# Kernel optimization log

Hardware: AMD Instinct MI355X
Metric: run time of the kernel (lower is better)

Reference implementation:

```python
import jax, jax.numpy as jnp
import numpy as np

_W1 = np.array([[[-1, 0, 0], [0, 1, 0], [0, 0, 0]],
                [[0, -1, 0], [0, 1, 0], [0, 0, 0]],
                [[0, 0, -1], [0, 1, 0], [0, 0, 0]],
                [[0, 0, 0], [-1, 1, 0], [0, 0, 0]]], dtype=np.float32).reshape(4, 1, 3, 3)
_W2 = _W1[:, :, ::-1, ::-1].copy()

BN_EPS = 1e-3  # YOLOX BaseConv BatchNorm eps
SHIFTS = (1, 3)


def _conv1x1(x, w, b=None):
    # x: (B,C,H,W), w: (O,C,1,1)
    y = jnp.einsum('bchw,oc->bohw', x, w[:, :, 0, 0])
    if b is not None:
        y = y + b[None, :, None, None]
    return y


def _grouped_dilated(x, w, d, groups):
    # 3x3 grouped conv, dilation d, 'same' padding (pad = d for 3x3)
    return jax.lax.conv_general_dilated(
        x, w, window_strides=(1, 1), padding=((d, d), (d, d)),
        rhs_dilation=(d, d), dimension_numbers=('NCHW', 'OIHW', 'NCHW'),
        feature_group_count=groups)


def setup_inputs() -> dict:
    key = jax.random.key(0)
    ks = jax.random.split(key, 6)
    B, C, H, W = 4, 128, 384, 384
    Cq = C // 4
    return {
        'cen': jax.random.normal(ks[0], (B, C, H, W), jnp.float32),
        'mas': jax.random.normal(ks[1], (B, 1, H, W), jnp.float32),
        'scales': jnp.zeros((4,), jnp.float32),
        'in_conv_w': jax.random.normal(ks[2], (Cq, C, 1, 1), jnp.float32) * 0.05,
        'in_conv_b': jnp.zeros((Cq,), jnp.float32),
        'base_w': jax.random.normal(ks[3], (Cq, Cq, 1, 1), jnp.float32) * 0.1,
        'bn_gamma': jnp.ones((Cq,), jnp.float32),
        'bn_beta': jnp.zeros((Cq,), jnp.float32),
        'bn_mean': jnp.zeros((Cq,), jnp.float32),
        'bn_var': jnp.ones((Cq,), jnp.float32),
        'out_w': jax.random.normal(ks[4], (1, Cq, 1, 1), jnp.float32) * 0.1,
        'out_b': jnp.zeros((1,), jnp.float32),
    }


def reference(cen, mas, scales, in_conv_w, in_conv_b, base_w,
              bn_gamma, bn_beta, bn_mean, bn_var, out_w, out_b):
    B, C, H, W = cen.shape
    Cq = C // 4
    k1 = jnp.asarray(np.tile(_W1, (Cq, 1, 1, 1)))  # (4*Cq,1,3,3)
    k2 = jnp.asarray(np.tile(_W2, (Cq, 1, 1, 1)))

    x = _conv1x1(cen, in_conv_w, in_conv_b)  # (B,Cq,H,W)
    outs = []
    for shift in SHIFTS:
        o1 = _grouped_dilated(x, k1, shift, Cq)  # (B,4*Cq,H,W)
        o2 = _grouped_dilated(x, k2, shift, Cq)
        o = (o1 * o2).reshape(B, Cq, 4, H, W).min(axis=2)
        outs.append(o)
    outs = jnp.stack(outs, axis=-1)  # (B,Cq,H,W,n_shifts)
    feat = jax.nn.relu(outs.max(axis=-1) + outs.mean(axis=-1))

    # out_conv = BaseConv(1x1, BN, SiLU) + Conv2d(Cq->1, 1x1)
    y = _conv1x1(feat, base_w)
    inv = jax.lax.rsqrt(bn_var + BN_EPS)
    y = (y - bn_mean[None, :, None, None]) * (bn_gamma * inv)[None, :, None, None] + bn_beta[None, :, None, None]
    y = jax.nn.silu(y)
    att = jax.nn.sigmoid(_conv1x1(y, out_w, out_b))  # (B,1,H,W)

    s = jax.nn.softmax(scales)
    m = jax.nn.sigmoid(mas)
    return cen * (att * m * s[0] + m * s[1] + s[2] * att + s[3])
```

## Files before the change

kernel.cpp:

```cpp
#include <hip/hip_runtime.h>

#define HH 384
#define WW 384
#define HWSZ (HH*WW)
#define CIN 128
#define CQ 32
#define NB 4
#define NPIX (NB*HWSZ)

typedef float __attribute__((ext_vector_type(2))) f2v;

__device__ __forceinline__ float sigmoidf_(float v){ return 1.0f/(1.0f + __expf(-v)); }

__global__ __launch_bounds__(256) void k_prep(
    const float* __restrict__ in_w, const float* __restrict__ base_w,
    const float* __restrict__ bn_g, const float* __restrict__ bn_b,
    const float* __restrict__ bn_m, const float* __restrict__ bn_v,
    const float* __restrict__ out_w, const float* __restrict__ out_b,
    const float* __restrict__ scales,
    float* __restrict__ wt, float* __restrict__ bt, float* __restrict__ prm){
  int t = threadIdx.x;
  for (int i = t; i < CIN*CQ; i += 256){ int c = i >> 5, o = i & 31; wt[i] = in_w[o*CIN + c]; }
  for (int i = t; i < CQ*CQ;  i += 256){ int c = i >> 5, o = i & 31; bt[i] = base_w[o*CQ + c]; }
  if (t < CQ){
    float inv = rsqrtf(bn_v[t] + 1e-3f);
    float g = bn_g[t]*inv;
    prm[t]      = g;
    prm[32 + t] = bn_b[t] - bn_m[t]*g;
    prm[64 + t] = out_w[t];
  }
  if (t == 0){
    float s0=scales[0], s1=scales[1], s2=scales[2], s3=scales[3];
    float mx = fmaxf(fmaxf(s0,s1), fmaxf(s2,s3));
    float e0=expf(s0-mx), e1=expf(s1-mx), e2=expf(s2-mx), e3=expf(s3-mx);
    float inv = 1.0f/(e0+e1+e2+e3);
    prm[96]=e0*inv; prm[97]=e1*inv; prm[98]=e2*inv; prm[99]=e3*inv;
    prm[100]=out_b[0];
  }
}

__global__ __launch_bounds__(256) void k_conv1(const float* __restrict__ cen,
    const float* __restrict__ wt, const float* __restrict__ bvec,
    float* __restrict__ x) {
  int t = threadIdx.x;
  int p0  = blockIdx.x * 512 + t*2;
  int b   = p0 / HWSZ;
  int pix = p0 - b*HWSZ;
  const float* cb = cen + (size_t)b*CIN*HWSZ + pix;
  float2 acc[CQ];
  #pragma unroll
  for (int o=0;o<CQ;o++){ float bb = bvec[o]; acc[o].x=bb; acc[o].y=bb; }

  f2v cur[4], nxt[4];
  #pragma unroll
  for (int k=0;k<4;k++) cur[k] = __builtin_nontemporal_load((const f2v*)(cb + (size_t)k*HWSZ));

  for (int c=0;c<CIN;c+=4){
    if (c+4 < CIN){
      #pragma unroll
      for (int k=0;k<4;k++) nxt[k] = __builtin_nontemporal_load((const f2v*)(cb + (size_t)(c+4+k)*HWSZ));
    }
    const float* wc = wt + c*CQ;
    #pragma unroll
    for (int k=0;k<4;k++){
      #pragma unroll
      for (int o=0;o<CQ;o++){
        float w = wc[k*CQ+o];
        acc[o].x = fmaf(cur[k].x, w, acc[o].x);
        acc[o].y = fmaf(cur[k].y, w, acc[o].y);
      }
    }
    #pragma unroll
    for (int k=0;k<4;k++) cur[k] = nxt[k];
  }
  float* xb = x + (size_t)b*CQ*HWSZ + pix;
  #pragma unroll
  for (int o=0;o<CQ;o++) *(float2*)(xb + (size_t)o*HWSZ) = acc[o];
}

#define TH 8
#define TW 64
#define LDSW 72
#define LDSN (14*LDSW)
#define GBX 6
#define GBY 48

__global__ __launch_bounds__(256) void k_att(const float* __restrict__ x,
    const float* __restrict__ cen, const float* __restrict__ mas,
    const float* __restrict__ bt, const float* __restrict__ prm,
    float* __restrict__ out) {
  __shared__ float tile[2][LDSN];
  int t = threadIdx.x;

  int gid = blockIdx.x;
  int b   = gid / (GBX*GBY);
  int rem = gid - b*(GBX*GBY);
  int ty  = rem / GBX;
  int tx  = rem - ty*GBX;
  int h0  = ty*TH, w0 = tx*TW;

  int soff[4]; float sval[4];
  #pragma unroll
  for (int j=0;j<4;j++){
    int i = t + j*256;
    int r = i / LDSW, cc = i - r*LDSW;
    int hh = h0 - 3 + r, wq = w0 - 3 + cc;
    bool ok = (i < LDSN) && (cc < 70) &&
              ((unsigned)hh < (unsigned)HH) && ((unsigned)wq < (unsigned)WW);
    soff[j] = ok ? (hh*WW + wq) : 0;
    sval[j] = ok ? 1.0f : 0.0f;
  }

  int rr = t >> 5;
  int ct = t & 31;
  const int R = 3 + rr, C = 3 + 2*ct;
  const int o_m3 = (R-3)*LDSW + C, o_m1 = (R-1)*LDSW + C,
            o_0  =  R   *LDSW + C, o_p1 = (R+1)*LDSW + C,
            o_p3 = (R+3)*LDSW + C;
  const float* xb = x + (size_t)b*CQ*HWSZ;

  float y0[CQ], y1[CQ];
  #pragma unroll
  for (int o=0;o<CQ;o++){ y0[o]=0.f; y1[o]=0.f; }

  float rg[4];
  #pragma unroll
  for (int j=0;j<4;j++) rg[j] = xb[soff[j]];

  #pragma unroll 2
  for (int c=0;c<CQ;c++){
    float* buf = tile[c&1];
    #pragma unroll
    for (int j=0;j<4;j++){
      int i = t + j*256;
      if (i < LDSN) buf[i] = sval[j]*rg[j];
    }
    float rg2[4];
    if (c+1 < CQ){
      const float* xn = xb + (size_t)(c+1)*HWSZ;
      #pragma unroll
      for (int j=0;j<4;j++) rg2[j] = xn[soff[j]];
    }
    __syncthreads();
    const float* p = buf;
    float2 m3a = *(const float2*)(p + o_m3 - 3);
    float  m3b0 = p[o_m3], m3b1 = p[o_m3 + 1];
    float2 m3c = *(const float2*)(p + o_m3 + 3);
    float2 m1a = *(const float2*)(p + o_m1 - 1);
    float2 m1b = *(const float2*)(p + o_m1 + 1);
    float2 z0  = *(const float2*)(p + o_0  - 3);
    float2 z1  = *(const float2*)(p + o_0  - 1);
    float2 z2  = *(const float2*)(p + o_0  + 1);
    float2 z3  = *(const float2*)(p + o_0  + 3);
    float2 p1a = *(const float2*)(p + o_p1 - 1);
    float2 p1b = *(const float2*)(p + o_p1 + 1);
    float2 p3a = *(const float2*)(p + o_p3 - 3);
    float  p3b0 = p[o_p3], p3b1 = p[o_p3 + 1];
    float2 p3c = *(const float2*)(p + o_p3 + 3);

    float xv = z1.y;
    float q0 = (xv-m1a.x)*(xv-p1b.x);
    float q1 = (xv-m1a.y)*(xv-p1a.y);
    float q2 = (xv-m1b.x)*(xv-p1a.x);
    float q3 = (xv-z1.x )*(xv-z2.x );
    float os0 = fminf(fminf(q0,q1),fminf(q2,q3));
    float r0 = (xv-m3a.x)*(xv-p3c.x);
    float r1 = (xv-m3b0 )*(xv-p3b0 );
    float r2 = (xv-m3c.x)*(xv-p3a.x);
    float r3 = (xv-z0.x )*(xv-z3.x );
    float os1 = fminf(fminf(r0,r1),fminf(r2,r3));
    float v0 = fmaxf(os0,os1) + 0.5f*(os0+os1);
    float fc0 = fmaxf(v0, 0.0f);

    float xw = z2.x;
    float u0 = (xw-m1a.y)*(xw-p1b.y);
    float u1 = (xw-m1b.x)*(xw-p1b.x);
    float u2 = (xw-m1b.y)*(xw-p1a.y);
    float u3 = (xw-z1.y )*(xw-z2.y );
    float ps0 = fminf(fminf(u0,u1),fminf(u2,u3));
    float s0 = (xw-m3a.y)*(xw-p3c.y);
    float s1 = (xw-m3b1 )*(xw-p3b1 );
    float s2 = (xw-m3c.y)*(xw-p3a.y);
    float s3 = (xw-z0.y )*(xw-z3.y );
    float ps1 = fminf(fminf(s0,s1),fminf(s2,s3));
    float v1 = fmaxf(ps0,ps1) + 0.5f*(ps0+ps1);
    float fc1 = fmaxf(v1, 0.0f);

    const float* wc = bt + c*CQ;
    #pragma unroll
    for (int o=0;o<CQ;o++){
      float w = wc[o];
      y0[o] = fmaf(fc0, w, y0[o]);
      y1[o] = fmaf(fc1, w, y1[o]);
    }
    #pragma unroll
    for (int j=0;j<4;j++) rg[j] = rg2[j];
  }

  float w0p=prm[96], w1p=prm[97], w2p=prm[98], w3p=prm[99], ob=prm[100];
  float lin0=ob, lin1=ob;
  #pragma unroll
  for (int o=0;o<CQ;o++){
    float g=prm[o], sh=prm[32+o], ow=prm[64+o];
    float yy0 = fmaf(y0[o], g, sh);
    float yy1 = fmaf(y1[o], g, sh);
    lin0 = fmaf(ow*yy0, sigmoidf_(yy0), lin0);
    lin1 = fmaf(ow*yy1, sigmoidf_(yy1), lin1);
  }
  float att0 = sigmoidf_(lin0);
  float att1 = sigmoidf_(lin1);

  int pix = (h0+rr)*WW + (w0 + 2*ct);
  float2 mm = *(const float2*)(mas + b*HWSZ + pix);
  float m0 = sigmoidf_(mm.x);
  float m1 = sigmoidf_(mm.y);
  float a0 = (att0*m0)*w0p + m0*w1p + att0*w2p + w3p;
  float a1 = (att1*m1)*w0p + m1*w1p + att1*w2p + w3p;

  const float* cb = cen + (size_t)b*CIN*HWSZ + pix;
  float*       od = out + (size_t)b*CIN*HWSZ + pix;
  #pragma unroll 8
  for (int c=0;c<CIN;c++){
    f2v v = __builtin_nontemporal_load((const f2v*)(cb + (size_t)c*HWSZ));
    v.x *= a0; v.y *= a1;
    __builtin_nontemporal_store(v, (f2v*)(od + (size_t)c*HWSZ));
  }
}

extern "C" void kernel_launch(void* const* d_in, const int* in_sizes, int n_in,
                              void* d_out, int out_size, void* d_ws, size_t ws_size,
                              hipStream_t stream) {
  const float* cen    = (const float*)d_in[0];
  const float* mas    = (const float*)d_in[1];
  const float* scales = (const float*)d_in[2];
  const float* in_w   = (const float*)d_in[3];
  const float* in_b   = (const float*)d_in[4];
  const float* base_w = (const float*)d_in[5];
  const float* bn_g   = (const float*)d_in[6];
  const float* bn_b   = (const float*)d_in[7];
  const float* bn_m   = (const float*)d_in[8];
  const float* bn_v   = (const float*)d_in[9];
  const float* out_w  = (const float*)d_in[10];
  const float* out_b  = (const float*)d_in[11];
  float* out = (float*)d_out;

  float* x   = (float*)d_ws;
  float* wt  = x  + (size_t)NB*CQ*HWSZ;
  float* bt  = wt + (size_t)CIN*CQ;
  float* prm = bt + (size_t)CQ*CQ;

  k_prep <<<1, 256, 0, stream>>>(in_w, base_w, bn_g, bn_b, bn_m, bn_v,
                                 out_w, out_b, scales, wt, bt, prm);
  k_conv1<<<NPIX/512, 256, 0, stream>>>(cen, wt, in_b, x);
  k_att  <<<NB*GBX*GBY, 256, 0, stream>>>(x, cen, mas, bt, prm, out);
}
```

Baseline: 605.9 us.

## Fuse input 1x1 conv into attention kernel, recomputing halo tile

Removes the separate 1x1 input-conv kernel and its 32-channel intermediate buffer in workspace. The fused kernel now computes the 128-to-32 channel conv directly for its own tile plus a 3-pixel halo, holding the results in registers and feeding them into the existing LDS dilated-difference stage. This saves the global write and re-read of the intermediate. In exchange, conv work is recomputed for the halo (about twice the useful pixels), cen is read with scalar gathers, and register pressure rises sharply from the 32x4 accumulator array.

```diff
diff --git a/kernel.cpp b/kernel.cpp
--- a/kernel.cpp
+++ b/kernel.cpp
@@ -6,7 +6,6 @@
 #define CIN 128
 #define CQ 32
 #define NB 4
-#define NPIX (NB*HWSZ)
 
 typedef float __attribute__((ext_vector_type(2))) f2v;
 
@@ -39,45 +38,6 @@
   }
 }
 
-__global__ __launch_bounds__(256) void k_conv1(const float* __restrict__ cen,
-    const float* __restrict__ wt, const float* __restrict__ bvec,
-    float* __restrict__ x) {
-  int t = threadIdx.x;
-  int p0  = blockIdx.x * 512 + t*2;
-  int b   = p0 / HWSZ;
-  int pix = p0 - b*HWSZ;
-  const float* cb = cen + (size_t)b*CIN*HWSZ + pix;
-  float2 acc[CQ];
-  #pragma unroll
-  for (int o=0;o<CQ;o++){ float bb = bvec[o]; acc[o].x=bb; acc[o].y=bb; }
-
-  f2v cur[4], nxt[4];
-  #pragma unroll
-  for (int k=0;k<4;k++) cur[k] = __builtin_nontemporal_load((const f2v*)(cb + (size_t)k*HWSZ));
-
-  for (int c=0;c<CIN;c+=4){
-    if (c+4 < CIN){
-      #pragma unroll
-      for (int k=0;k<4;k++) nxt[k] = __builtin_nontemporal_load((const f2v*)(cb + (size_t)(c+4+k)*HWSZ));
-    }
-    const float* wc = wt + c*CQ;
-    #pragma unroll
-    for (int k=0;k<4;k++){
-      #pragma unroll
-      for (int o=0;o<CQ;o++){
-        float w = wc[k*CQ+o];
-        acc[o].x = fmaf(cur[k].x, w, acc[o].x);
-        acc[o].y = fmaf(cur[k].y, w, acc[o].y);
-      }
-    }
-    #pragma unroll
-    for (int k=0;k<4;k++) cur[k] = nxt[k];
-  }
-  float* xb = x + (size_t)b*CQ*HWSZ + pix;
-  #pragma unroll
-  for (int o=0;o<CQ;o++) *(float2*)(xb + (size_t)o*HWSZ) = acc[o];
-}
-
 #define TH 8
 #define TW 64
 #define LDSW 72
@@ -85,8 +45,9 @@
 #define GBX 6
 #define GBY 48
 
-__global__ __launch_bounds__(256) void k_att(const float* __restrict__ x,
-    const float* __restrict__ cen, const float* __restrict__ mas,
+__global__ __launch_bounds__(256) void k_fused(const float* __restrict__ cen,
+    const float* __restrict__ mas,
+    const float* __restrict__ wt, const float* __restrict__ bvec,
     const float* __restrict__ bt, const float* __restrict__ prm,
     float* __restrict__ out) {
   __shared__ float tile[2][LDSN];
@@ -111,35 +72,56 @@
     sval[j] = ok ? 1.0f : 0.0f;
   }
 
+  const float* cb = cen + (size_t)b*CIN*HWSZ;
+
+  float acc[CQ][4];
+  #pragma unroll
+  for (int o=0;o<CQ;o++){
+    float bb = bvec[o];
+    #pragma unroll
+    for (int j=0;j<4;j++) acc[o][j] = bb;
+  }
+  float cva[4], cvb[4], nva[4], nvb[4];
+  #pragma unroll
+  for (int j=0;j<4;j++){ cva[j] = cb[soff[j]]; cvb[j] = cb[HWSZ + soff[j]]; }
+  for (int ci=0; ci<CIN; ci+=2){
+    if (ci+2 < CIN){
+      const float* c2 = cb + (size_t)(ci+2)*HWSZ;
+      #pragma unroll
+      for (int j=0;j<4;j++){ nva[j] = c2[soff[j]]; nvb[j] = c2[HWSZ + soff[j]]; }
+    }
+    const float* wa = wt + ci*CQ;
+    #pragma unroll
+    for (int o=0;o<CQ;o++){
+      float wA = wa[o], wB = wa[CQ+o];
+      #pragma unroll
+      for (int j=0;j<4;j++){
+        acc[o][j] = fmaf(cva[j], wA, acc[o][j]);
+        acc[o][j] = fmaf(cvb[j], wB, acc[o][j]);
+      }
+    }
+    #pragma unroll
+    for (int j=0;j<4;j++){ cva[j] = nva[j]; cvb[j] = nvb[j]; }
+  }
+
   int rr = t >> 5;
   int ct = t & 31;
   const int R = 3 + rr, C = 3 + 2*ct;
   const int o_m3 = (R-3)*LDSW + C, o_m1 = (R-1)*LDSW + C,
             o_0  =  R   *LDSW + C, o_p1 = (R+1)*LDSW + C,
             o_p3 = (R+3)*LDSW + C;
-  const float* xb = x + (size_t)b*CQ*HWSZ;
 
   float y0[CQ], y1[CQ];
   #pragma unroll
   for (int o=0;o<CQ;o++){ y0[o]=0.f; y1[o]=0.f; }
 
-  float rg[4];
-  #pragma unroll
-  for (int j=0;j<4;j++) rg[j] = xb[soff[j]];
-
-  #pragma unroll 2
+  #pragma unroll
   for (int c=0;c<CQ;c++){
     float* buf = tile[c&1];
     #pragma unroll
     for (int j=0;j<4;j++){
       int i = t + j*256;
-      if (i < LDSN) buf[i] = sval[j]*rg[j];
-    }
-    float rg2[4];
-    if (c+1 < CQ){
-      const float* xn = xb + (size_t)(c+1)*HWSZ;
-      #pragma unroll
-      for (int j=0;j<4;j++) rg2[j] = xn[soff[j]];
+      if (i < LDSN) buf[i] = sval[j]*acc[c][j];
     }
     __syncthreads();
     const float* p = buf;
@@ -193,8 +175,6 @@
       y0[o] = fmaf(fc0, w, y0[o]);
       y1[o] = fmaf(fc1, w, y1[o]);
     }
-    #pragma unroll
-    for (int j=0;j<4;j++) rg[j] = rg2[j];
   }
 
   float w0p=prm[96], w1p=prm[97], w2p=prm[98], w3p=prm[99], ob=prm[100];
@@ -217,11 +197,11 @@
   float a0 = (att0*m0)*w0p + m0*w1p + att0*w2p + w3p;
   float a1 = (att1*m1)*w0p + m1*w1p + att1*w2p + w3p;
 
-  const float* cb = cen + (size_t)b*CIN*HWSZ + pix;
+  const float* cs = cb + pix;
   float*       od = out + (size_t)b*CIN*HWSZ + pix;
   #pragma unroll 8
   for (int c=0;c<CIN;c++){
-    f2v v = __builtin_nontemporal_load((const f2v*)(cb + (size_t)c*HWSZ));
+    f2v v = __builtin_nontemporal_load((const f2v*)(cs + (size_t)c*HWSZ));
     v.x *= a0; v.y *= a1;
     __builtin_nontemporal_store(v, (f2v*)(od + (size_t)c*HWSZ));
   }
@@ -244,13 +224,11 @@
   const float* out_b  = (const float*)d_in[11];
   float* out = (float*)d_out;
 
-  float* x   = (float*)d_ws;
-  float* wt  = x  + (size_t)NB*CQ*HWSZ;
+  float* wt  = (float*)d_ws;
   float* bt  = wt + (size_t)CIN*CQ;
   float* prm = bt + (size_t)CQ*CQ;
 
   k_prep <<<1, 256, 0, stream>>>(in_w, base_w, bn_g, bn_b, bn_m, bn_v,
                                  out_w, out_b, scales, wt, bt, prm);
-  k_conv1<<<NPIX/512, 256, 0, stream>>>(cen, wt, in_b, x);
-  k_att  <<<NB*GBX*GBY, 256, 0, stream>>>(x, cen, mas, bt, prm, out);
+  k_fused<<<NB*GBX*GBY, 256, 0, stream>>>(cen, mas, wt, in_b, bt, prm, out);
 }
```

New measurement: 932.5 us. 53.9% more time.
